# Kernel optimization log

Hardware: AMD Instinct MI355X
Metric: run time of the kernel (lower is better)

The kernel has to match this reference:

```python
import jax, jax.numpy as jnp
import numpy as np

D_MODEL, HEAD_DIM = 1024, 128

def setup_inputs() -> dict:
    key = jax.random.key(0)
    kx, kq, kk, kv = jax.random.split(key, 4)
    x = jax.random.normal(kx, (4, 4096, D_MODEL), dtype=jnp.float32)
    s = 1.0 / np.sqrt(D_MODEL)
    Wq = jax.random.normal(kq, (D_MODEL, HEAD_DIM), dtype=jnp.float32) * s
    Wk = jax.random.normal(kk, (D_MODEL, HEAD_DIM), dtype=jnp.float32) * s
    Wv = jax.random.normal(kv, (D_MODEL, HEAD_DIM), dtype=jnp.float32) * s
    return {"x": x, "Wq": Wq, "Wk": Wk, "Wv": Wv}

def reference(x, Wq, Wk, Wv):
    # x: [b, s, d_model]; Wq/Wk/Wv: [d_model, head_dim]
    q = jnp.einsum('bsd,dh->bsh', x, Wq)
    k = jnp.einsum('bsd,dh->bsh', x, Wk)
    v = jnp.einsum('bsd,dh->bsh', x, Wv)
    seq = x.shape[1]
    scale = 1.0 / jnp.sqrt(jnp.asarray(q.shape[-1], q.dtype))
    scores = jnp.einsum('bqh,bkh->bqk', q, k) * scale  # [b, s, s]
    causal = jnp.tril(jnp.ones((seq, seq), dtype=bool))
    scores = jnp.where(causal, scores, jnp.asarray(-jnp.inf, scores.dtype))
    attn = jax.nn.softmax(scores, axis=-1)
    return jnp.einsum('bqk,bkh->bqh', attn, v)
```

## Files before the change

### kernel.cpp

```cpp
#include <hip/hip_runtime.h>
#include <hip/hip_bf16.h>
#include <math.h>

#define D_MODEL 1024
#define HD 128
#define SEQ 4096

typedef __bf16 bf16x8 __attribute__((ext_vector_type(8)));
typedef float f32x4 __attribute__((ext_vector_type(4)));
typedef unsigned int u32;
typedef u32 u32x4 __attribute__((ext_vector_type(4)));

__device__ __forceinline__ unsigned short f2bf(float f) {
    union { float f; u32 u; } c; c.f = f;
    u32 u = c.u;
    u = (u + 0x7fffu + ((u >> 16) & 1u)) >> 16;
    return (unsigned short)u;
}
__device__ __forceinline__ u32 pk2(float a, float b) {
    __hip_bfloat162 h = __float22bfloat162_rn(make_float2(a, b));
    union { __hip_bfloat162 h; u32 u; } c; c.h = h; return c.u;
}
__device__ __forceinline__ void dma16(void* lds, const void* g) {
    __builtin_amdgcn_global_load_lds(
        (const __attribute__((address_space(1))) u32*)g,
        (__attribute__((address_space(3))) u32*)lds, 16, 0, 0);
}
__device__ __forceinline__ void drain_dma()  { __builtin_amdgcn_s_waitcnt(0x0F70); }

__global__ __launch_bounds__(256)
void wt_kernel(const float* __restrict__ Wq, const float* __restrict__ Wk,
               const float* __restrict__ Wv, unsigned short* __restrict__ Wt) {
    __shared__ float wsf[64][129];
    const int t = threadIdx.x;
    const int k0 = blockIdx.x * 64;
    const int mat = blockIdx.y;
    const float* W = (mat == 0) ? Wq : (mat == 1) ? Wk : Wv;
    const float sc = (mat == 0) ? (0.08838834764831845f * 1.4426950408889634f) : 1.0f;
    {
        const int r = t >> 2, c = (t & 3) * 32;
        const float* src = W + (size_t)(k0 + r) * HD + c;
        #pragma unroll
        for (int j = 0; j < 32; j += 4)
            *reinterpret_cast<f32x4*>(&wsf[r][c + j]) = *reinterpret_cast<const f32x4*>(src + j);
    }
    __syncthreads();
    const int n = t >> 1, ks = (t & 1) * 32;
    u32 ow[16];
    #pragma unroll
    for (int j = 0; j < 16; ++j)
        ow[j] = pk2(wsf[ks + 2 * j][n] * sc, wsf[ks + 2 * j + 1][n] * sc);
    unsigned short* dst = Wt + (size_t)(mat * HD + n) * D_MODEL + k0 + ks;
    #pragma unroll
    for (int j = 0; j < 4; ++j)
        *reinterpret_cast<u32x4*>(dst + j * 8) = (u32x4){ow[4*j], ow[4*j+1], ow[4*j+2], ow[4*j+3]};
}

__global__ __launch_bounds__(1024, 1)
void proj_kernel(const float* __restrict__ x, const unsigned short* __restrict__ Wt,
                 unsigned short* __restrict__ Qb, unsigned short* __restrict__ Kb,
                 unsigned short* __restrict__ Vt) {
    __shared__ __align__(1024) char ps[131072];
    const int t = threadIdx.x;
    const int w = t >> 6, l = t & 63, li = l & 15, g2 = l >> 4;
    const int mh = w >> 2, nq = w & 3;
    const int rowbase = blockIdx.x * 64;

    const int lr = l >> 3, lg = l & 7;
    const int cg = lg ^ lr;
    const int wn_add = (cg >> 2) * 192;
    const int wkq = (cg & 3) * 8;

    auto stage = [&](int it) {
        const int k0 = it * 32;
        const int buf = it & 3;
        char* xb = ps + buf * 8192;
        char* wbuf = ps + 32768 + buf * 24576;
        if (w < 8) {
            dma16(xb + w * 1024,
                  x + (size_t)(rowbase + w * 8 + lr) * D_MODEL + k0 + cg * 4);
            dma16(wbuf + w * 1024,
                  Wt + (size_t)(w * 8 + lr + wn_add) * D_MODEL + k0 + wkq);
        } else {
            const int j0 = 8 + (w - 8) * 2;
            dma16(wbuf + j0 * 1024,
                  Wt + (size_t)(j0 * 8 + lr + wn_add) * D_MODEL + k0 + wkq);
            dma16(wbuf + (j0 + 1) * 1024,
                  Wt + (size_t)((j0 + 1) * 8 + lr + wn_add) * D_MODEL + k0 + wkq);
        }
    };

    f32x4 acc[6];
    #pragma unroll
    for (int nt = 0; nt < 6; ++nt) acc[nt] = (f32x4){0.f, 0.f, 0.f, 0.f};

    stage(0); stage(1); stage(2);
    for (int it = 0; it < 32; ++it) {
        if (it < 30)       asm volatile("s_waitcnt vmcnt(4) lgkmcnt(0)" ::: "memory");
        else if (it == 30) asm volatile("s_waitcnt vmcnt(2) lgkmcnt(0)" ::: "memory");
        else               asm volatile("s_waitcnt vmcnt(0) lgkmcnt(0)" ::: "memory");
        __builtin_amdgcn_s_barrier();
        if (it + 3 < 32) stage(it + 3);

        const char* xb = ps + (it & 3) * 8192;
        const char* wb = ps + 32768 + (it & 3) * 24576;

        bf16x8 bf[6];
        #pragma unroll
        for (int nt = 0; nt < 6; ++nt) {
            int r = (nq & 1) * 96 + nt * 16 + li;
            bf[nt] = *reinterpret_cast<const bf16x8*>(
                wb + r * 128 + ((((nq >> 1) * 4 + g2) ^ (li & 7)) * 16));
        }
        {
            int row = mh * 16 + li;
            int p0 = ((2 * g2) ^ (li & 7)) * 16;
            f32x4 x0 = *reinterpret_cast<const f32x4*>(xb + row * 128 + p0);
            f32x4 x1 = *reinterpret_cast<const f32x4*>(xb + row * 128 + (p0 ^ 16));
            union { u32 d[4]; bf16x8 v; } cva;
            cva.d[0] = pk2(x0[0], x0[1]); cva.d[1] = pk2(x0[2], x0[3]);
            cva.d[2] = pk2(x1[0], x1[1]); cva.d[3] = pk2(x1[2], x1[3]);
            bf16x8 af = cva.v;
            #pragma unroll
            for (int nt = 0; nt < 6; ++nt)
                acc[nt] = __builtin_amdgcn_mfma_f32_16x16x32_bf16(af, bf[nt], acc[nt], 0, 0, 0);
        }
    }

    #pragma unroll
    for (int nt = 0; nt < 6; ++nt) {
        const int c0 = nq * 96 + nt * 16;
        const int m0 = rowbase + mh * 16 + g2 * 4;
        if (c0 < 256) {
            unsigned short* P = (c0 < 128) ? Qb : Kb;
            const int col = (c0 < 128 ? c0 : c0 - 128) + li;
            #pragma unroll
            for (int r = 0; r < 4; ++r)
                P[(size_t)(m0 + r) * HD + col] = f2bf(acc[nt][r]);
        } else {
            const int d = c0 - 256 + li;
            const int b_ = m0 >> 12, s_ = m0 & 4095;
            ushort4 s4;
            s4.x = f2bf(acc[nt][0]); s4.y = f2bf(acc[nt][1]);
            s4.z = f2bf(acc[nt][2]); s4.w = f2bf(acc[nt][3]);
            *reinterpret_cast<ushort4*>(&Vt[((size_t)b_ * HD + d) * SEQ + s_]) = s4;
        }
    }
}

__global__ __launch_bounds__(512, 2)
void attn_kernel(const unsigned short* __restrict__ Qb, const unsigned short* __restrict__ Kb,
                 const unsigned short* __restrict__ Vt, float* __restrict__ outO,
                 unsigned short* __restrict__ Obf, float* __restrict__ Lbuf) {
    __shared__ __align__(1024) char smem[81920];
    const int t = threadIdx.x;
    const int w = t >> 6, l = t & 63, li = l & 15, g2 = l >> 4;
    const int qh = w >> 1, kh = w & 1;
    const int b = blockIdx.x & 3;
    const int u = blockIdx.x >> 2;
    const int g = 31 - (u >> 2);
    const int c = u & 3;
    const int R = 2 * g + 2;
    const int ts = (c * R) >> 2, te = ((c + 1) * R) >> 2;
    const int q0 = g * 128;
    const size_t rowb = (size_t)b * SEQ;
    const int koff = kh * 32;

    const unsigned short* KbB = Kb + rowb * HD;
    const unsigned short* VtB = Vt + (size_t)b * HD * SEQ;
    const int vgran = ((l & 7) ^ (l >> 3)) * 8;

    auto stage = [&](int it, char* base) {
        const int j0 = it * 64;
        #pragma unroll
        for (int j = 0; j < 2; ++j) {
            int rK = w * 8 + 4 * j + (l >> 4);
            dma16(base + (w * 8 + 4 * j) * 256,
                  KbB + (size_t)(j0 + rK) * 128 + (((l & 15) ^ (rK & 7)) * 8));
            int rV = w * 16 + 8 * j + (l >> 3);
            dma16(base + 16384 + (w * 16 + 8 * j) * 128,
                  VtB + (size_t)rV * SEQ + j0 + vgran);
        }
    };

    bf16x8 qf[2][4];
    #pragma unroll
    for (int qt = 0; qt < 2; ++qt)
        #pragma unroll
        for (int ks = 0; ks < 4; ++ks)
            qf[qt][ks] = *reinterpret_cast<const bf16x8*>(
                Qb + (rowb + q0 + qh * 32 + qt * 16 + li) * HD + ks * 32 + g2 * 8);

    f32x4 acco[2][8];
    #pragma unroll
    for (int qt = 0; qt < 2; ++qt)
        #pragma unroll
        for (int dt = 0; dt < 8; ++dt) acco[qt][dt] = (f32x4){0.f, 0.f, 0.f, 0.f};
    float ls[2] = {0.f, 0.f};

    const int gV = ((4 * kh + g2) ^ (li & 7)) * 16;

    if (ts < te) stage(ts, smem);
    for (int it = ts; it < te; ++it) {
        char* cbuf = smem + ((it - ts) & 1) * 32768;
        char* nbuf = smem + (((it - ts) & 1) ^ 1) * 32768;
        drain_dma();
        __syncthreads();
        if (it + 1 < te) stage(it + 1, nbuf);

        f32x4 accs[2][2];
        #pragma unroll
        for (int qt = 0; qt < 2; ++qt)
            #pragma unroll
            for (int kt = 0; kt < 2; ++kt) accs[qt][kt] = (f32x4){0.f, 0.f, 0.f, 0.f};
        #pragma unroll
        for (int kt = 0; kt < 2; ++kt) {
            const char* kb = cbuf + (koff + kt * 16 + li) * 256;
            #pragma unroll
            for (int ks = 0; ks < 4; ++ks) {
                bf16x8 kf = *reinterpret_cast<const bf16x8*>(kb + (((4 * ks + g2) ^ (li & 7)) * 16));
                accs[0][kt] = __builtin_amdgcn_mfma_f32_16x16x32_bf16(kf, qf[0][ks], accs[0][kt], 0, 0, 0);
                accs[1][kt] = __builtin_amdgcn_mfma_f32_16x16x32_bf16(kf, qf[1][ks], accs[1][kt], 0, 0, 0);
            }
        }

        const int dmask = it - 2 * g;
        #pragma unroll
        for (int qt = 0; qt < 2; ++qt) {
            const int prow = qh * 32 + qt * 16 + li;
            #pragma unroll
            for (int kt = 0; kt < 2; ++kt) {
                float p[4];
                #pragma unroll
                for (int r = 0; r < 4; ++r) {
                    float s = accs[qt][kt][r];
                    if (dmask >= 0 && (dmask * 64 + koff + kt * 16 + g2 * 4 + r > prow))
                        s = -INFINITY;
                    p[r] = __builtin_amdgcn_exp2f(s - 16.0f);
                    ls[qt] += p[r];
                }
                union { u32 d[2]; uint2 v; } pw;
                pw.d[0] = pk2(p[0], p[1]); pw.d[1] = pk2(p[2], p[3]);
                int gr = (kh * 4 + kt * 2 + (g2 >> 1)) ^ (prow & 7);
                *reinterpret_cast<uint2*>(
                    smem + 65536 + prow * 128 + gr * 16 + (g2 & 1) * 8) = pw.v;
            }
        }

        bf16x8 pb[2];
        #pragma unroll
        for (int qt = 0; qt < 2; ++qt) {
            const int prow = qh * 32 + qt * 16 + li;
            pb[qt] = *reinterpret_cast<const bf16x8*>(
                smem + 65536 + prow * 128 + (((kh * 4 + g2) ^ (prow & 7)) * 16));
        }
        #pragma unroll
        for (int dt = 0; dt < 8; ++dt) {
            bf16x8 va = *reinterpret_cast<const bf16x8*>(cbuf + 16384 + (dt * 16 + li) * 128 + gV);
            acco[0][dt] = __builtin_amdgcn_mfma_f32_16x16x32_bf16(va, pb[0], acco[0][dt], 0, 0, 0);
            acco[1][dt] = __builtin_amdgcn_mfma_f32_16x16x32_bf16(va, pb[1], acco[1][dt], 0, 0, 0);
        }
    }

    #pragma unroll
    for (int qt = 0; qt < 2; ++qt) {
        ls[qt] += __shfl_xor(ls[qt], 16);
        ls[qt] += __shfl_xor(ls[qt], 32);
    }

    float (*Osum)[132] = (float(*)[132])smem;
    float* Lsh = (float*)(smem + 67584);
    __syncthreads();
    if (l < 16) {
        Lsh[kh * 128 + qh * 32 + l]      = ls[0];
        Lsh[kh * 128 + qh * 32 + 16 + l] = ls[1];
    }
    if (kh == 0) {
        #pragma unroll
        for (int qt = 0; qt < 2; ++qt)
            #pragma unroll
            for (int dt = 0; dt < 8; ++dt)
                *reinterpret_cast<f32x4*>(
                    &Osum[qh * 32 + qt * 16 + li][dt * 16 + g2 * 4]) = acco[qt][dt];
    }
    __syncthreads();
    if (kh == 1) {
        #pragma unroll
        for (int qt = 0; qt < 2; ++qt)
            #pragma unroll
            for (int dt = 0; dt < 8; ++dt) {
                f32x4* p = reinterpret_cast<f32x4*>(
                    &Osum[qh * 32 + qt * 16 + li][dt * 16 + g2 * 4]);
                f32x4 v = *p;
                #pragma unroll
                for (int j = 0; j < 4; ++j) v[j] += acco[qt][dt][j];
                *p = v;
            }
    }
    __syncthreads();

    if (t < 128)
        Lbuf[(size_t)c * 16384 + rowb + q0 + t] = Lsh[t] + Lsh[128 + t];
    #pragma unroll
    for (int k = 0; k < 8; ++k) {
        int idx = t + k * 512;
        int row = idx >> 5, col = (idx & 31) * 4;
        f32x4 o = *reinterpret_cast<const f32x4*>(&Osum[row][col]);
        size_t grow = rowb + q0 + row;
        if (c == 3) {
            *reinterpret_cast<f32x4*>(&outO[grow * HD + col]) = o;
        } else {
            union { u32 d[2]; uint2 v; } pkd;
            pkd.d[0] = pk2(o[0], o[1]); pkd.d[1] = pk2(o[2], o[3]);
            *reinterpret_cast<uint2*>(&Obf[(size_t)c * 2097152 + grow * HD + col]) = pkd.v;
        }
    }
}

__global__ __launch_bounds__(256)
void merge_kernel(float* __restrict__ outO, const unsigned short* __restrict__ Obf,
                  const float* __restrict__ Lbuf) {
    int tid = blockIdx.x * 256 + threadIdx.x;
    #pragma unroll
    for (int k = 0; k < 4; ++k) {
        int idx = tid + k * 131072;
        int row = idx >> 5, col = (idx & 31) * 4;
        float lsum = Lbuf[row] + Lbuf[16384 + row] + Lbuf[32768 + row] + Lbuf[49152 + row];
        float inv = 1.f / lsum;
        f32x4 o = *reinterpret_cast<const f32x4*>(&outO[(size_t)row * HD + col]);
        #pragma unroll
        for (int cc = 0; cc < 3; ++cc) {
            ushort4 uu = *reinterpret_cast<const ushort4*>(
                &Obf[(size_t)cc * 2097152 + (size_t)row * HD + col]);
            union { u32 u; float f; } a, b2, c2, d2;
            a.u = (u32)uu.x << 16; b2.u = (u32)uu.y << 16;
            c2.u = (u32)uu.z << 16; d2.u = (u32)uu.w << 16;
            o[0] += a.f; o[1] += b2.f; o[2] += c2.f; o[3] += d2.f;
        }
        #pragma unroll
        for (int j = 0; j < 4; ++j) o[j] *= inv;
        *reinterpret_cast<f32x4*>(&outO[(size_t)row * HD + col]) = o;
    }
}

extern "C" void kernel_launch(void* const* d_in, const int* in_sizes, int n_in,
                              void* d_out, int out_size, void* d_ws, size_t ws_size,
                              hipStream_t stream) {
    const float* x  = (const float*)d_in[0];
    const float* Wq = (const float*)d_in[1];
    const float* Wk = (const float*)d_in[2];
    const float* Wv = (const float*)d_in[3];
    float* out = (float*)d_out;

    char* ws = (char*)d_ws;
    unsigned short* Qb  = (unsigned short*)(ws);
    unsigned short* Kb  = (unsigned short*)(ws + ((size_t)4  << 20));
    unsigned short* Vt  = (unsigned short*)(ws + ((size_t)8  << 20));
    unsigned short* Wt  = (unsigned short*)(ws + ((size_t)12 << 20));
    unsigned short* Obf = (unsigned short*)(ws + ((size_t)13 << 20));
    float*          Lb  = (float*)(ws + ((size_t)25 << 20));

    wt_kernel   <<<dim3(16, 3), dim3(256), 0, stream>>>(Wq, Wk, Wv, Wt);
    proj_kernel <<<dim3(256),   dim3(1024), 0, stream>>>(x, Wt, Qb, Kb, Vt);
    attn_kernel <<<dim3(512),   dim3(512), 0, stream>>>(Qb, Kb, Vt, out, Obf, Lb);
    merge_kernel<<<dim3(512),   dim3(256), 0, stream>>>(out, Obf, Lb);
}
```

Baseline: 163.7 us.

## Fuse split-K merge into attention kernel via last-block atomic counter

Removes the separate merge kernel launch. Each attention block bumps a per-(batch, query-tile) atomic counter after writing its partial output, and the last of the four splits merges the partials and normalizes in place. Counters are zeroed in the weight-transpose kernel each call. This saves a launch and a full pass over the partial buffers, at the cost of threadfences, an atomic per block, and a merge tail that runs on whichever block finishes last.

```diff
diff --git a/kernel.cpp b/kernel.cpp
--- a/kernel.cpp
+++ b/kernel.cpp
@@ -30,9 +30,11 @@
 
 __global__ __launch_bounds__(256)
 void wt_kernel(const float* __restrict__ Wq, const float* __restrict__ Wk,
-               const float* __restrict__ Wv, unsigned short* __restrict__ Wt) {
+               const float* __restrict__ Wv, unsigned short* __restrict__ Wt,
+               unsigned int* __restrict__ ctr) {
     __shared__ float wsf[64][129];
     const int t = threadIdx.x;
+    if (blockIdx.x == 0 && blockIdx.y == 0 && t < 128) ctr[t] = 0u;
     const int k0 = blockIdx.x * 64;
     const int mat = blockIdx.y;
     const float* W = (mat == 0) ? Wq : (mat == 1) ? Wk : Wv;
@@ -151,7 +153,8 @@
 __global__ __launch_bounds__(512, 2)
 void attn_kernel(const unsigned short* __restrict__ Qb, const unsigned short* __restrict__ Kb,
                  const unsigned short* __restrict__ Vt, float* __restrict__ outO,
-                 unsigned short* __restrict__ Obf, float* __restrict__ Lbuf) {
+                 unsigned short* __restrict__ Obf, float* __restrict__ Lbuf,
+                 unsigned int* __restrict__ ctr) {
     __shared__ __align__(1024) char smem[81920];
     const int t = threadIdx.x;
     const int w = t >> 6, l = t & 63, li = l & 15, g2 = l >> 4;
@@ -315,31 +318,39 @@
             *reinterpret_cast<uint2*>(&Obf[(size_t)c * 2097152 + grow * HD + col]) = pkd.v;
         }
     }
-}
-
-__global__ __launch_bounds__(256)
-void merge_kernel(float* __restrict__ outO, const unsigned short* __restrict__ Obf,
-                  const float* __restrict__ Lbuf) {
-    int tid = blockIdx.x * 256 + threadIdx.x;
-    #pragma unroll
-    for (int k = 0; k < 4; ++k) {
-        int idx = tid + k * 131072;
-        int row = idx >> 5, col = (idx & 31) * 4;
-        float lsum = Lbuf[row] + Lbuf[16384 + row] + Lbuf[32768 + row] + Lbuf[49152 + row];
-        float inv = 1.f / lsum;
-        f32x4 o = *reinterpret_cast<const f32x4*>(&outO[(size_t)row * HD + col]);
-        #pragma unroll
-        for (int cc = 0; cc < 3; ++cc) {
-            ushort4 uu = *reinterpret_cast<const ushort4*>(
-                &Obf[(size_t)cc * 2097152 + (size_t)row * HD + col]);
-            union { u32 u; float f; } a, b2, c2, d2;
-            a.u = (u32)uu.x << 16; b2.u = (u32)uu.y << 16;
-            c2.u = (u32)uu.z << 16; d2.u = (u32)uu.w << 16;
-            o[0] += a.f; o[1] += b2.f; o[2] += c2.f; o[3] += d2.f;
-        }
-        #pragma unroll
-        for (int j = 0; j < 4; ++j) o[j] *= inv;
-        *reinterpret_cast<f32x4*>(&outO[(size_t)row * HD + col]) = o;
+
+    __threadfence();
+    __syncthreads();
+    volatile unsigned int* flag = (volatile unsigned int*)(smem + 69632);
+    if (t == 0) {
+        unsigned int old = atomicAdd(&ctr[(b << 5) + g], 1u);
+        *flag = (old == 3u) ? 1u : 0u;
+    }
+    __syncthreads();
+    if (*flag) {
+        __threadfence();
+        #pragma unroll
+        for (int k = 0; k < 8; ++k) {
+            int idx = t + k * 512;
+            int row = idx >> 5, col = (idx & 31) * 4;
+            size_t grow = rowb + q0 + row;
+            float lsum = Lbuf[grow] + Lbuf[16384 + grow] +
+                         Lbuf[32768 + grow] + Lbuf[49152 + grow];
+            float inv = 1.f / lsum;
+            f32x4 o = *reinterpret_cast<const f32x4*>(&outO[grow * HD + col]);
+            #pragma unroll
+            for (int cc = 0; cc < 3; ++cc) {
+                ushort4 uu = *reinterpret_cast<const ushort4*>(
+                    &Obf[(size_t)cc * 2097152 + grow * HD + col]);
+                union { u32 u; float f; } a, b2, c2, d2;
+                a.u = (u32)uu.x << 16; b2.u = (u32)uu.y << 16;
+                c2.u = (u32)uu.z << 16; d2.u = (u32)uu.w << 16;
+                o[0] += a.f; o[1] += b2.f; o[2] += c2.f; o[3] += d2.f;
+            }
+            #pragma unroll
+            for (int j = 0; j < 4; ++j) o[j] *= inv;
+            *reinterpret_cast<f32x4*>(&outO[grow * HD + col]) = o;
+        }
     }
 }
 
@@ -359,9 +370,9 @@
     unsigned short* Wt  = (unsigned short*)(ws + ((size_t)12 << 20));
     unsigned short* Obf = (unsigned short*)(ws + ((size_t)13 << 20));
     float*          Lb  = (float*)(ws + ((size_t)25 << 20));
-
-    wt_kernel   <<<dim3(16, 3), dim3(256), 0, stream>>>(Wq, Wk, Wv, Wt);
+    unsigned int*   Ct  = (unsigned int*)(ws + ((size_t)26 << 20));
+
+    wt_kernel   <<<dim3(16, 3), dim3(256),  0, stream>>>(Wq, Wk, Wv, Wt, Ct);
     proj_kernel <<<dim3(256),   dim3(1024), 0, stream>>>(x, Wt, Qb, Kb, Vt);
-    attn_kernel <<<dim3(512),   dim3(512), 0, stream>>>(Qb, Kb, Vt, out, Obf, Lb);
-    merge_kernel<<<dim3(512),   dim3(256), 0, stream>>>(out, Obf, Lb);
-}
+    attn_kernel <<<dim3(512),   dim3(512),  0, stream>>>(Qb, Kb, Vt, out, Obf, Lb, Ct);
+}
```

Result: slower. 317.3 us (+93.8%).

## Split causal attention KV range into fixed-size chunks instead of four equal parts

Applied to the files above, without the earlier changes.

Each 128-row query tile used to be split into four chunks of equal KV length, so early tiles had tiny chunks and late tiles had large ones. Now every chunk covers at most eight 64-key iterations, so the number of chunks per tile grows with its causal length. That gives 576 blocks of roughly equal work, ordered longest-first. The merge kernel now loops over a variable number of partial results per row, and the workspace for the bf16 partial outputs is enlarged to hold up to eight chunks. The costs are more partial outputs to write and merge for late tiles, and a small index-decoding loop at kernel start.

```diff
diff --git a/kernel.cpp b/kernel.cpp
--- a/kernel.cpp
+++ b/kernel.cpp
@@ -157,11 +157,21 @@
     const int w = t >> 6, l = t & 63, li = l & 15, g2 = l >> 4;
     const int qh = w >> 1, kh = w & 1;
     const int b = blockIdx.x & 3;
-    const int u = blockIdx.x >> 2;
-    const int g = 31 - (u >> 2);
-    const int c = u & 3;
+    int j = 143 - (int)(blockIdx.x >> 2);
+    int g = 0, ci = 0;
+    {
+        int pre = 0;
+        #pragma unroll
+        for (int a = 0; a < 8; ++a) {
+            int cnt = 4 * (a + 1);
+            if (j < pre + cnt) { int off = j - pre; g = 4 * a + off / (a + 1); ci = off % (a + 1); break; }
+            pre += cnt;
+        }
+    }
+    const int nch = (g >> 2) + 1;
     const int R = 2 * g + 2;
-    const int ts = (c * R) >> 2, te = ((c + 1) * R) >> 2;
+    const int ts = ci * 8, te = (ts + 8 < R) ? ts + 8 : R;
+    const bool fin = (ci == nch - 1);
     const int q0 = g * 128;
     const size_t rowb = (size_t)b * SEQ;
     const int koff = kh * 32;
@@ -173,12 +183,12 @@
     auto stage = [&](int it, char* base) {
         const int j0 = it * 64;
         #pragma unroll
-        for (int j = 0; j < 2; ++j) {
-            int rK = w * 8 + 4 * j + (l >> 4);
-            dma16(base + (w * 8 + 4 * j) * 256,
+        for (int jj = 0; jj < 2; ++jj) {
+            int rK = w * 8 + 4 * jj + (l >> 4);
+            dma16(base + (w * 8 + 4 * jj) * 256,
                   KbB + (size_t)(j0 + rK) * 128 + (((l & 15) ^ (rK & 7)) * 8));
-            int rV = w * 16 + 8 * j + (l >> 3);
-            dma16(base + 16384 + (w * 16 + 8 * j) * 128,
+            int rV = w * 16 + 8 * jj + (l >> 3);
+            dma16(base + 16384 + (w * 16 + 8 * jj) * 128,
                   VtB + (size_t)rV * SEQ + j0 + vgran);
         }
     };
@@ -293,26 +303,26 @@
                     &Osum[qh * 32 + qt * 16 + li][dt * 16 + g2 * 4]);
                 f32x4 v = *p;
                 #pragma unroll
-                for (int j = 0; j < 4; ++j) v[j] += acco[qt][dt][j];
+                for (int jj = 0; jj < 4; ++jj) v[jj] += acco[qt][dt][jj];
                 *p = v;
             }
     }
     __syncthreads();
 
     if (t < 128)
-        Lbuf[(size_t)c * 16384 + rowb + q0 + t] = Lsh[t] + Lsh[128 + t];
+        Lbuf[(size_t)ci * 16384 + rowb + q0 + t] = Lsh[t] + Lsh[128 + t];
     #pragma unroll
     for (int k = 0; k < 8; ++k) {
         int idx = t + k * 512;
         int row = idx >> 5, col = (idx & 31) * 4;
         f32x4 o = *reinterpret_cast<const f32x4*>(&Osum[row][col]);
         size_t grow = rowb + q0 + row;
-        if (c == 3) {
+        if (fin) {
             *reinterpret_cast<f32x4*>(&outO[grow * HD + col]) = o;
         } else {
             union { u32 d[2]; uint2 v; } pkd;
             pkd.d[0] = pk2(o[0], o[1]); pkd.d[1] = pk2(o[2], o[3]);
-            *reinterpret_cast<uint2*>(&Obf[(size_t)c * 2097152 + grow * HD + col]) = pkd.v;
+            *reinterpret_cast<uint2*>(&Obf[(size_t)ci * 2097152 + grow * HD + col]) = pkd.v;
         }
     }
 }
@@ -325,11 +335,13 @@
     for (int k = 0; k < 4; ++k) {
         int idx = tid + k * 131072;
         int row = idx >> 5, col = (idx & 31) * 4;
-        float lsum = Lbuf[row] + Lbuf[16384 + row] + Lbuf[32768 + row] + Lbuf[49152 + row];
+        int g = (row & 4095) >> 7;
+        int nch = (g >> 2) + 1;
+        float lsum = 0.f;
+        for (int ci = 0; ci < nch; ++ci) lsum += Lbuf[(size_t)ci * 16384 + row];
         float inv = 1.f / lsum;
         f32x4 o = *reinterpret_cast<const f32x4*>(&outO[(size_t)row * HD + col]);
-        #pragma unroll
-        for (int cc = 0; cc < 3; ++cc) {
+        for (int cc = 0; cc < nch - 1; ++cc) {
             ushort4 uu = *reinterpret_cast<const ushort4*>(
                 &Obf[(size_t)cc * 2097152 + (size_t)row * HD + col]);
             union { u32 u; float f; } a, b2, c2, d2;
@@ -338,7 +350,7 @@
             o[0] += a.f; o[1] += b2.f; o[2] += c2.f; o[3] += d2.f;
         }
         #pragma unroll
-        for (int j = 0; j < 4; ++j) o[j] *= inv;
+        for (int jj = 0; jj < 4; ++jj) o[jj] *= inv;
         *reinterpret_cast<f32x4*>(&outO[(size_t)row * HD + col]) = o;
     }
 }
@@ -358,10 +370,10 @@
     unsigned short* Vt  = (unsigned short*)(ws + ((size_t)8  << 20));
     unsigned short* Wt  = (unsigned short*)(ws + ((size_t)12 << 20));
     unsigned short* Obf = (unsigned short*)(ws + ((size_t)13 << 20));
-    float*          Lb  = (float*)(ws + ((size_t)25 << 20));
-
-    wt_kernel   <<<dim3(16, 3), dim3(256), 0, stream>>>(Wq, Wk, Wv, Wt);
+    float*          Lb  = (float*)(ws + ((size_t)41 << 20));
+
+    wt_kernel   <<<dim3(16, 3), dim3(256),  0, stream>>>(Wq, Wk, Wv, Wt);
     proj_kernel <<<dim3(256),   dim3(1024), 0, stream>>>(x, Wt, Qb, Kb, Vt);
-    attn_kernel <<<dim3(512),   dim3(512), 0, stream>>>(Qb, Kb, Vt, out, Obf, Lb);
-    merge_kernel<<<dim3(512),   dim3(256), 0, stream>>>(out, Obf, Lb);
-}
+    attn_kernel <<<dim3(576),   dim3(512),  0, stream>>>(Qb, Kb, Vt, out, Obf, Lb);
+    merge_kernel<<<dim3(512),   dim3(256),  0, stream>>>(out, Obf, Lb);
+}
```

Measured after the change: 189.2 us. 1.16x slower.
